# Kernel tuning notes

Hardware: AMD Instinct MI355X
Metric: run time of the kernel (lower is better)

The kernel has to match this reference:

```python
import jax, jax.numpy as jnp
import numpy as np

B, T, D, H, K = 2, 1024, 1024, 4096, 8


def setup_inputs() -> dict:
    key = jax.random.key(0)
    ks = jax.random.split(key, 5)
    x = jax.random.normal(ks[0], (B, T, D), dtype=jnp.float32)
    # hard one-hot routing weights per token (no learned router)
    expert_ids = jax.random.randint(ks[1], (B, T), 0, K)
    combine_weights = jax.nn.one_hot(expert_ids, K, dtype=jnp.float32)
    scale_in = 1.0 / np.sqrt(D)
    scale_h = 1.0 / np.sqrt(H)
    wg = jax.random.normal(ks[2], (K, D, H), dtype=jnp.float32) * scale_in
    wu = jax.random.normal(ks[3], (K, D, H), dtype=jnp.float32) * scale_in
    wd = jax.random.normal(ks[4], (K, H, D), dtype=jnp.float32) * scale_h
    return {"x": x, "combine_weights": combine_weights, "wg": wg, "wu": wu, "wd": wd}


def reference(x, combine_weights, wg, wu, wd):
    # Each expert is a SwiGLU FFN: down( silu(gate(x)) * up(x) ).
    # Dense baseline: every token runs through all K experts (as in source).
    g = jnp.einsum('btd,kdh->btkh', x, wg)          # [B,T,K,H]
    u = jnp.einsum('btd,kdh->btkh', x, wu)          # [B,T,K,H]
    h = jax.nn.silu(g) * u                          # [B,T,K,H]
    expert_outs = jnp.einsum('btkh,khd->btkd', h, wd)  # [B,T,K,D]
    y = jnp.einsum('btk,btkd->btd', combine_weights, expert_outs)
    return y.astype(x.dtype)
```

## Files before the change

kernel.cpp:

```cpp
#include <hip/hip_runtime.h>
#include <hip/hip_bf16.h>

typedef __attribute__((ext_vector_type(8))) short bf16x8;
typedef __attribute__((ext_vector_type(4))) float f32x4;
typedef unsigned short u16;

#define NTOK 2048
#define DDIM 1024
#define HDIM 4096
#define KEXP 8

#define BM 320
#define BK 64
#define NDESC 16

__device__ __forceinline__ u16 f2bf(float f) {
  __hip_bfloat16 b = __float2bfloat16(f);
  union { __hip_bfloat16 b; u16 u; } c; c.b = b; return c.u;
}
__device__ __forceinline__ unsigned pk2(float a, float b) {
  return (unsigned)f2bf(a) | ((unsigned)f2bf(b) << 16);
}

#define BAR() do { \
  asm volatile("s_waitcnt lgkmcnt(0)" ::: "memory"); \
  __builtin_amdgcn_sched_barrier(0); \
  __builtin_amdgcn_s_barrier(); \
  __builtin_amdgcn_sched_barrier(0); \
} while (0)

__global__ void route_kernel(const float* __restrict__ cw, int* __restrict__ offs,
                             int* __restrict__ perm, float* __restrict__ wsel,
                             int* __restrict__ desc) {
  __shared__ int cnt[KEXP];
  __shared__ int base[KEXP];
  const int t = threadIdx.x;
  if (t < KEXP) cnt[t] = 0;
  __syncthreads();
  int eid[8]; float wv[8];
  #pragma unroll
  for (int i = 0; i < 8; i++) {
    const int tok = t * 8 + i;
    const float* p = cw + tok * KEXP;
    int best = 0; float bw = p[0];
    #pragma unroll
    for (int k = 1; k < KEXP; k++) { float v = p[k]; if (v > bw) { bw = v; best = k; } }
    eid[i] = best; wv[i] = bw;
    atomicAdd(&cnt[best], 1);
  }
  __syncthreads();
  if (t == 0) {
    int s = 0, nd = 0;
    for (int k = 0; k < KEXP; k++) {
      const int ck = cnt[k];
      base[k] = s; offs[k] = s;
      for (int m0 = 0; m0 < ck && nd < NDESC; m0 += BM)
        desc[nd++] = (k << 12) | (s + m0);
      s += ck;
    }
    offs[KEXP] = s;
    for (; nd < NDESC; nd++) desc[nd] = -1;
  }
  __syncthreads();
  #pragma unroll
  for (int i = 0; i < 8; i++) {
    const int tok = t * 8 + i;
    const int pos = atomicAdd(&base[eid[i]], 1);
    perm[pos] = tok;
    wsel[pos] = wv[i];
  }
}

__global__ void gather_x(const float* __restrict__ x, const int* __restrict__ perm,
                         u16* __restrict__ Xb) {
  const int slot = blockIdx.x;
  const int tok = perm[slot];
  const int t = threadIdx.x;
  float4 v = ((const float4*)(x + (size_t)tok * DDIM))[t];
  ushort4 o; o.x = f2bf(v.x); o.y = f2bf(v.y); o.z = f2bf(v.z); o.w = f2bf(v.w);
  ((ushort4*)(Xb + (size_t)slot * DDIM))[t] = o;
}

__global__ __launch_bounds__(1024, 4) void gemm_swiglu(
    const u16* __restrict__ Xb,
    const float* __restrict__ wg, const float* __restrict__ wu,
    const int* __restrict__ offs, const int* __restrict__ desc,
    u16* __restrict__ Hb) {
  __shared__ u16 As[2][BM * 64];
  __shared__ u16 Bs[2][2][64 * 64];

  const int d = desc[blockIdx.y];
  if (d < 0) return;
  const int e = d >> 12;
  const int slot0 = d & 0xFFF;
  const int Msub = offs[e + 1] - slot0;
  const int mceil = min(BM, (Msub + 15) & ~15);
  const int n0 = blockIdx.x * 64;

  const int t = threadIdx.x;
  const int lane = t & 63;
  const int W = t >> 6;
  const int wm = W >> 2;
  const int wn = W & 3;
  const int l15 = lane & 15;
  const int lhi = lane >> 4;
  const int fm_lim = min(5, max(0, (Msub - wm * 80 + 15) >> 4));

  const int a_row = t >> 1;
  const bool do_a = (t < 640) && (a_row < mceil);
  const int a_c0 = (t & 1) * 4;
  const u16* a_src = Xb + (size_t)min(slot0 + a_row, NTOK - 1) * DDIM + a_c0 * 8;
  const int a_swz = a_row & 7;

  const int tb = t & 511;
  const int matsel = t >> 9;
  const float* b_base = (matsel ? wu : wg) + (size_t)e * DDIM * HDIM;
  const int b_n = tb & 63;
  const int b_c = tb >> 6;
  const float* b_src = b_base + (size_t)(b_c * 8) * HDIM + n0 + b_n;
  const int b_off = b_n * 64 + ((b_c ^ (b_n & 7)) << 3);

  float bR[8];
  uint4 aT0, aT1, aT2, aT3;
  f32x4 accg[5] = {};
  f32x4 accu[5] = {};

  #define AISSUE(tile) if (do_a) { const uint4* p_ = (const uint4*)(a_src + (tile) * BK); \
    aT0 = p_[0]; aT1 = p_[1]; aT2 = p_[2]; aT3 = p_[3]; }
  #define AWRITE(buf) if (do_a) { u16* base_ = &As[buf][a_row * 64]; \
    *(uint4*)(base_ + (((a_c0 + 0) ^ a_swz) << 3)) = aT0; \
    *(uint4*)(base_ + (((a_c0 + 1) ^ a_swz) << 3)) = aT1; \
    *(uint4*)(base_ + (((a_c0 + 2) ^ a_swz) << 3)) = aT2; \
    *(uint4*)(base_ + (((a_c0 + 3) ^ a_swz) << 3)) = aT3; }
  #define LOADB(tile) { const float* p_ = b_src + (size_t)(tile) * BK * HDIM; \
    _Pragma("unroll") for (int j = 0; j < 8; j++) bR[j] = p_[(size_t)j * HDIM]; }
  #define WRITEB(buf) { uint4 w_; \
    w_.x = pk2(bR[0], bR[1]); w_.y = pk2(bR[2], bR[3]); \
    w_.z = pk2(bR[4], bR[5]); w_.w = pk2(bR[6], bR[7]); \
    *(uint4*)(&Bs[buf][matsel][b_off]) = w_; }
  #define COMPUTE(buf) { _Pragma("unroll") for (int ks = 0; ks < 2; ks++) { \
      const int cx_ = (((ks << 2) + lhi) ^ (l15 & 7)) << 3; \
      bf16x8 bg_ = *(const bf16x8*)(&Bs[buf][0][(wn * 16 + l15) * 64] + cx_); \
      bf16x8 bu_ = *(const bf16x8*)(&Bs[buf][1][(wn * 16 + l15) * 64] + cx_); \
      _Pragma("unroll") for (int fm = 0; fm < 5; fm++) { \
        if (fm < fm_lim) { \
          bf16x8 af_ = *(const bf16x8*)(&As[buf][(wm * 80 + fm * 16 + l15) * 64] + cx_); \
          accg[fm] = __builtin_amdgcn_mfma_f32_16x16x32_bf16(af_, bg_, accg[fm], 0, 0, 0); \
          accu[fm] = __builtin_amdgcn_mfma_f32_16x16x32_bf16(af_, bu_, accu[fm], 0, 0, 0); } } } }

  LOADB(0);
  AISSUE(0);
  WRITEB(0);
  LOADB(1);
  AWRITE(0);
  BAR();

  #pragma unroll 1
  for (int it = 0; it < 16; it += 2) {
    if (it + 1 < 16) AISSUE(it + 1);
    __builtin_amdgcn_sched_barrier(0);
    COMPUTE(0);
    if (it + 1 < 16) {
      WRITEB(1);
      if (it + 2 < 16) LOADB(it + 2);
      AWRITE(1);
    }
    BAR();
    if (it + 2 < 16) AISSUE(it + 2);
    __builtin_amdgcn_sched_barrier(0);
    COMPUTE(1);
    if (it + 2 < 16) {
      WRITEB(0);
      if (it + 3 < 16) LOADB(it + 3);
      AWRITE(0);
    }
    BAR();
  }
  #undef AISSUE
  #undef AWRITE
  #undef LOADB
  #undef WRITEB
  #undef COMPUTE

  #pragma unroll
  for (int fm = 0; fm < 5; fm++) {
    #pragma unroll
    for (int i = 0; i < 4; i++) {
      const int row = wm * 80 + fm * 16 + lhi * 4 + i;
      if (row < Msub) {
        const float g = accg[fm][i];
        const float u = accu[fm][i];
        const float h = (g / (1.0f + __expf(-g))) * u;
        Hb[(size_t)(slot0 + row) * HDIM + n0 + wn * 16 + l15] = f2bf(h);
      }
    }
  }
}

__global__ __launch_bounds__(1024, 4) void gemm_down(
    const u16* __restrict__ Hb, const float* __restrict__ wd,
    const int* __restrict__ offs, const int* __restrict__ desc,
    const int* __restrict__ perm, const float* __restrict__ wsel,
    float* __restrict__ y) {
  __shared__ u16 As[2][BM * 64];
  __shared__ u16 Bs[2][128 * 64];

  const int d = desc[blockIdx.y];
  if (d < 0) return;
  const int e = d >> 12;
  const int slot0 = d & 0xFFF;
  const int Msub = offs[e + 1] - slot0;
  const int mceil = min(BM, (Msub + 15) & ~15);
  const int n0 = blockIdx.x * 128;
  const int kbase = blockIdx.z * (HDIM / 4);

  const float* Wd = wd + (size_t)e * HDIM * DDIM;

  const int t = threadIdx.x;
  const int lane = t & 63;
  const int W = t >> 6;
  const int wm = W >> 2;
  const int wn = W & 3;
  const int l15 = lane & 15;
  const int lhi = lane >> 4;
  const int fm_lim = min(5, max(0, (Msub - wm * 80 + 15) >> 4));

  const int a_row = t >> 1;
  const bool do_a = (t < 640) && (a_row < mceil);
  const int a_c0 = (t & 1) * 4;
  const u16* a_src = Hb + (size_t)min(slot0 + a_row, NTOK - 1) * HDIM + kbase + a_c0 * 8;
  const int a_swz = a_row & 7;

  const int b_n = t & 127;
  const int b_c = t >> 7;
  const float* b_src = Wd + (size_t)(kbase + b_c * 8) * DDIM + n0 + b_n;
  const int b_off = b_n * 64 + ((b_c ^ (b_n & 7)) << 3);

  float bR[8];
  uint4 aT0, aT1, aT2, aT3;
  f32x4 acc[5][2] = {};

  #define AISSUE(tile) if (do_a) { const uint4* p_ = (const uint4*)(a_src + (tile) * BK); \
    aT0 = p_[0]; aT1 = p_[1]; aT2 = p_[2]; aT3 = p_[3]; }
  #define AWRITE(buf) if (do_a) { u16* base_ = &As[buf][a_row * 64]; \
    *(uint4*)(base_ + (((a_c0 + 0) ^ a_swz) << 3)) = aT0; \
    *(uint4*)(base_ + (((a_c0 + 1) ^ a_swz) << 3)) = aT1; \
    *(uint4*)(base_ + (((a_c0 + 2) ^ a_swz) << 3)) = aT2; \
    *(uint4*)(base_ + (((a_c0 + 3) ^ a_swz) << 3)) = aT3; }
  #define LOADB(tile) { const float* p_ = b_src + (size_t)(tile) * BK * DDIM; \
    _Pragma("unroll") for (int j = 0; j < 8; j++) bR[j] = p_[(size_t)j * DDIM]; }
  #define WRITEB(buf) { uint4 w_; \
    w_.x = pk2(bR[0], bR[1]); w_.y = pk2(bR[2], bR[3]); \
    w_.z = pk2(bR[4], bR[5]); w_.w = pk2(bR[6], bR[7]); \
    *(uint4*)(&Bs[buf][b_off]) = w_; }
  #define COMPUTE(buf) { _Pragma("unroll") for (int ks = 0; ks < 2; ks++) { \
      const int cx_ = (((ks << 2) + lhi) ^ (l15 & 7)) << 3; \
      bf16x8 bf0_ = *(const bf16x8*)(&Bs[buf][(wn * 32 + l15) * 64] + cx_); \
      bf16x8 bf1_ = *(const bf16x8*)(&Bs[buf][(wn * 32 + 16 + l15) * 64] + cx_); \
      _Pragma("unroll") for (int fm = 0; fm < 5; fm++) { \
        if (fm < fm_lim) { \
          bf16x8 af_ = *(const bf16x8*)(&As[buf][(wm * 80 + fm * 16 + l15) * 64] + cx_); \
          acc[fm][0] = __builtin_amdgcn_mfma_f32_16x16x32_bf16(af_, bf0_, acc[fm][0], 0, 0, 0); \
          acc[fm][1] = __builtin_amdgcn_mfma_f32_16x16x32_bf16(af_, bf1_, acc[fm][1], 0, 0, 0); } } } }

  LOADB(0);
  AISSUE(0);
  WRITEB(0);
  LOADB(1);
  AWRITE(0);
  BAR();

  #pragma unroll 1
  for (int it = 0; it < 16; it += 2) {
    if (it + 1 < 16) AISSUE(it + 1);
    __builtin_amdgcn_sched_barrier(0);
    COMPUTE(0);
    if (it + 1 < 16) {
      WRITEB(1);
      if (it + 2 < 16) LOADB(it + 2);
      AWRITE(1);
    }
    BAR();
    if (it + 2 < 16) AISSUE(it + 2);
    __builtin_amdgcn_sched_barrier(0);
    COMPUTE(1);
    if (it + 2 < 16) {
      WRITEB(0);
      if (it + 3 < 16) LOADB(it + 3);
      AWRITE(0);
    }
    BAR();
  }
  #undef AISSUE
  #undef AWRITE
  #undef LOADB
  #undef WRITEB
  #undef COMPUTE

  #pragma unroll
  for (int fm = 0; fm < 5; fm++) {
    #pragma unroll
    for (int i = 0; i < 4; i++) {
      const int row = wm * 80 + fm * 16 + lhi * 4 + i;
      if (row < Msub) {
        const int slot = slot0 + row;
        const int tok = perm[slot];
        const float w = wsel[slot];
        const size_t base = (size_t)tok * DDIM + n0 + wn * 32;
        atomicAdd(y + base + l15, acc[fm][0][i] * w);
        atomicAdd(y + base + 16 + l15, acc[fm][1][i] * w);
      }
    }
  }
}

extern "C" void kernel_launch(void* const* d_in, const int* in_sizes, int n_in,
                              void* d_out, int out_size, void* d_ws, size_t ws_size,
                              hipStream_t stream) {
  const float* x  = (const float*)d_in[0];
  const float* cw = (const float*)d_in[1];
  const float* wg = (const float*)d_in[2];
  const float* wu = (const float*)d_in[3];
  const float* wd = (const float*)d_in[4];
  float* y = (float*)d_out;

  char* ws = (char*)d_ws;
  int* offs   = (int*)ws;
  int* desc   = (int*)(ws + 64);
  int* perm   = (int*)(ws + 128);
  float* wsel = (float*)(ws + 128 + NTOK * 4);
  u16* Xb = (u16*)(ws + 32768);
  u16* Hb = (u16*)(ws + 32768 + (size_t)NTOK * DDIM * 2);

  hipMemsetAsync(d_out, 0, (size_t)NTOK * DDIM * sizeof(float), stream);
  route_kernel<<<1, 256, 0, stream>>>(cw, offs, perm, wsel, desc);
  gather_x<<<NTOK, 256, 0, stream>>>(x, perm, Xb);
  gemm_swiglu<<<dim3(HDIM / 64, NDESC), 1024, 0, stream>>>(Xb, wg, wu, offs, desc, Hb);
  gemm_down<<<dim3(DDIM / 128, NDESC, 4), 1024, 0, stream>>>(Hb, wd, offs, desc, perm, wsel, y);
}
```

Measured before the change: 151.6 us.

## Load A tiles directly global-to-LDS with pre-swizzled activation layouts

Replaces the register-staged A-tile loads (global to VGPR, then ds_write) in both GEMM kernels with global_load_lds direct copies into shared memory. Since direct LDS loads cannot apply a per-row swizzle on write, the producers (gather_x and the SwiGLU epilogue) now store activations with the XOR swizzle already applied in global memory, and the compute reads use a slot-based swizzle. Barriers now wait on vmcnt so the async copies are complete before use. This is meant to cut VGPR pressure and LDS write instructions, in exchange for coupling the global layout to the kernel's tile shape and relying on precise vmcnt counts for correctness.

```diff
diff --git a/kernel.cpp b/kernel.cpp
--- a/kernel.cpp
+++ b/kernel.cpp
@@ -22,8 +22,8 @@
   return (unsigned)f2bf(a) | ((unsigned)f2bf(b) << 16);
 }
 
-#define BAR() do { \
-  asm volatile("s_waitcnt lgkmcnt(0)" ::: "memory"); \
+#define BARV(N) do { \
+  asm volatile("s_waitcnt lgkmcnt(0) vmcnt(" #N ")" ::: "memory"); \
   __builtin_amdgcn_sched_barrier(0); \
   __builtin_amdgcn_s_barrier(); \
   __builtin_amdgcn_sched_barrier(0); \
@@ -76,9 +76,12 @@
   const int slot = blockIdx.x;
   const int tok = perm[slot];
   const int t = threadIdx.x;
+  const int s7 = slot & 7;
   float4 v = ((const float4*)(x + (size_t)tok * DDIM))[t];
   ushort4 o; o.x = f2bf(v.x); o.y = f2bf(v.y); o.z = f2bf(v.z); o.w = f2bf(v.w);
-  ((ushort4*)(Xb + (size_t)slot * DDIM))[t] = o;
+  const int c = t >> 1;
+  const int cp = (c & ~7) | ((c & 7) ^ s7);
+  *(ushort4*)(Xb + (size_t)slot * DDIM + cp * 8 + (t & 1) * 4) = o;
 }
 
 __global__ __launch_bounds__(1024, 4) void gemm_swiglu(
@@ -94,7 +97,6 @@
   const int e = d >> 12;
   const int slot0 = d & 0xFFF;
   const int Msub = offs[e + 1] - slot0;
-  const int mceil = min(BM, (Msub + 15) & ~15);
   const int n0 = blockIdx.x * 64;
 
   const int t = threadIdx.x;
@@ -105,12 +107,7 @@
   const int l15 = lane & 15;
   const int lhi = lane >> 4;
   const int fm_lim = min(5, max(0, (Msub - wm * 80 + 15) >> 4));
-
-  const int a_row = t >> 1;
-  const bool do_a = (t < 640) && (a_row < mceil);
-  const int a_c0 = (t & 1) * 4;
-  const u16* a_src = Xb + (size_t)min(slot0 + a_row, NTOK - 1) * DDIM + a_c0 * 8;
-  const int a_swz = a_row & 7;
+  const int asw = (slot0 + l15) & 7;
 
   const int tb = t & 511;
   const int matsel = t >> 9;
@@ -121,17 +118,20 @@
   const int b_off = b_n * 64 + ((b_c ^ (b_n & 7)) << 3);
 
   float bR[8];
-  uint4 aT0, aT1, aT2, aT3;
   f32x4 accg[5] = {};
   f32x4 accu[5] = {};
 
-  #define AISSUE(tile) if (do_a) { const uint4* p_ = (const uint4*)(a_src + (tile) * BK); \
-    aT0 = p_[0]; aT1 = p_[1]; aT2 = p_[2]; aT3 = p_[3]; }
-  #define AWRITE(buf) if (do_a) { u16* base_ = &As[buf][a_row * 64]; \
-    *(uint4*)(base_ + (((a_c0 + 0) ^ a_swz) << 3)) = aT0; \
-    *(uint4*)(base_ + (((a_c0 + 1) ^ a_swz) << 3)) = aT1; \
-    *(uint4*)(base_ + (((a_c0 + 2) ^ a_swz) << 3)) = aT2; \
-    *(uint4*)(base_ + (((a_c0 + 3) ^ a_swz) << 3)) = aT3; }
+  #define AGLOAD(tile, buf) if (t < 640) { \
+    _Pragma("unroll") for (int j = 0; j < 4; j++) { \
+      const int q_ = j * 640 + t; \
+      const int row_ = q_ >> 3; \
+      const u16* src_ = Xb + (size_t)min(slot0 + row_, NTOK - 1) * DDIM \
+                        + (tile) * BK + (q_ & 7) * 8; \
+      __builtin_amdgcn_global_load_lds( \
+        (const __attribute__((address_space(1))) unsigned int*)src_, \
+        (__attribute__((address_space(3))) unsigned int*)(&As[buf][0] + q_ * 8), \
+        16, 0, 0); \
+    } }
   #define LOADB(tile) { const float* p_ = b_src + (size_t)(tile) * BK * HDIM; \
     _Pragma("unroll") for (int j = 0; j < 8; j++) bR[j] = p_[(size_t)j * HDIM]; }
   #define WRITEB(buf) { uint4 w_; \
@@ -139,45 +139,42 @@
     w_.z = pk2(bR[4], bR[5]); w_.w = pk2(bR[6], bR[7]); \
     *(uint4*)(&Bs[buf][matsel][b_off]) = w_; }
   #define COMPUTE(buf) { _Pragma("unroll") for (int ks = 0; ks < 2; ks++) { \
-      const int cx_ = (((ks << 2) + lhi) ^ (l15 & 7)) << 3; \
-      bf16x8 bg_ = *(const bf16x8*)(&Bs[buf][0][(wn * 16 + l15) * 64] + cx_); \
-      bf16x8 bu_ = *(const bf16x8*)(&Bs[buf][1][(wn * 16 + l15) * 64] + cx_); \
+      const int cb_ = (((ks << 2) + lhi) ^ (l15 & 7)) << 3; \
+      const int ca_ = (((ks << 2) + lhi) ^ asw) << 3; \
+      bf16x8 bg_ = *(const bf16x8*)(&Bs[buf][0][(wn * 16 + l15) * 64] + cb_); \
+      bf16x8 bu_ = *(const bf16x8*)(&Bs[buf][1][(wn * 16 + l15) * 64] + cb_); \
       _Pragma("unroll") for (int fm = 0; fm < 5; fm++) { \
         if (fm < fm_lim) { \
-          bf16x8 af_ = *(const bf16x8*)(&As[buf][(wm * 80 + fm * 16 + l15) * 64] + cx_); \
+          bf16x8 af_ = *(const bf16x8*)(&As[buf][(wm * 80 + fm * 16 + l15) * 64] + ca_); \
           accg[fm] = __builtin_amdgcn_mfma_f32_16x16x32_bf16(af_, bg_, accg[fm], 0, 0, 0); \
           accu[fm] = __builtin_amdgcn_mfma_f32_16x16x32_bf16(af_, bu_, accu[fm], 0, 0, 0); } } } }
 
   LOADB(0);
-  AISSUE(0);
+  AGLOAD(0, 0);
   WRITEB(0);
   LOADB(1);
-  AWRITE(0);
-  BAR();
+  BARV(8);
 
   #pragma unroll 1
   for (int it = 0; it < 16; it += 2) {
-    if (it + 1 < 16) AISSUE(it + 1);
+    if (it + 1 < 16) AGLOAD(it + 1, 1);
     __builtin_amdgcn_sched_barrier(0);
     COMPUTE(0);
     if (it + 1 < 16) {
       WRITEB(1);
       if (it + 2 < 16) LOADB(it + 2);
-      AWRITE(1);
-    }
-    BAR();
-    if (it + 2 < 16) AISSUE(it + 2);
+    }
+    if (it + 2 < 16) BARV(8); else BARV(0);
+    if (it + 2 < 16) AGLOAD(it + 2, 0);
     __builtin_amdgcn_sched_barrier(0);
     COMPUTE(1);
     if (it + 2 < 16) {
       WRITEB(0);
       if (it + 3 < 16) LOADB(it + 3);
-      AWRITE(0);
-    }
-    BAR();
-  }
-  #undef AISSUE
-  #undef AWRITE
+    }
+    if (it + 3 < 16) BARV(8); else BARV(0);
+  }
+  #undef AGLOAD
   #undef LOADB
   #undef WRITEB
   #undef COMPUTE
@@ -191,7 +188,8 @@
         const float g = accg[fm][i];
         const float u = accu[fm][i];
         const float h = (g / (1.0f + __expf(-g))) * u;
-        Hb[(size_t)(slot0 + row) * HDIM + n0 + wn * 16 + l15] = f2bf(h);
+        const int s7 = (slot0 + row) & 7;
+        Hb[(size_t)(slot0 + row) * HDIM + ((n0 + wn * 16 + l15) ^ (s7 << 3))] = f2bf(h);
       }
     }
   }
@@ -210,7 +208,6 @@
   const int e = d >> 12;
   const int slot0 = d & 0xFFF;
   const int Msub = offs[e + 1] - slot0;
-  const int mceil = min(BM, (Msub + 15) & ~15);
   const int n0 = blockIdx.x * 128;
   const int kbase = blockIdx.z * (HDIM / 4);
 
@@ -224,12 +221,7 @@
   const int l15 = lane & 15;
   const int lhi = lane >> 4;
   const int fm_lim = min(5, max(0, (Msub - wm * 80 + 15) >> 4));
-
-  const int a_row = t >> 1;
-  const bool do_a = (t < 640) && (a_row < mceil);
-  const int a_c0 = (t & 1) * 4;
-  const u16* a_src = Hb + (size_t)min(slot0 + a_row, NTOK - 1) * HDIM + kbase + a_c0 * 8;
-  const int a_swz = a_row & 7;
+  const int asw = (slot0 + l15) & 7;
 
   const int b_n = t & 127;
   const int b_c = t >> 7;
@@ -237,16 +229,19 @@
   const int b_off = b_n * 64 + ((b_c ^ (b_n & 7)) << 3);
 
   float bR[8];
-  uint4 aT0, aT1, aT2, aT3;
   f32x4 acc[5][2] = {};
 
-  #define AISSUE(tile) if (do_a) { const uint4* p_ = (const uint4*)(a_src + (tile) * BK); \
-    aT0 = p_[0]; aT1 = p_[1]; aT2 = p_[2]; aT3 = p_[3]; }
-  #define AWRITE(buf) if (do_a) { u16* base_ = &As[buf][a_row * 64]; \
-    *(uint4*)(base_ + (((a_c0 + 0) ^ a_swz) << 3)) = aT0; \
-    *(uint4*)(base_ + (((a_c0 + 1) ^ a_swz) << 3)) = aT1; \
-    *(uint4*)(base_ + (((a_c0 + 2) ^ a_swz) << 3)) = aT2; \
-    *(uint4*)(base_ + (((a_c0 + 3) ^ a_swz) << 3)) = aT3; }
+  #define AGLOAD(tile, buf) if (t < 640) { \
+    _Pragma("unroll") for (int j = 0; j < 4; j++) { \
+      const int q_ = j * 640 + t; \
+      const int row_ = q_ >> 3; \
+      const u16* src_ = Hb + (size_t)min(slot0 + row_, NTOK - 1) * HDIM \
+                        + kbase + (tile) * BK + (q_ & 7) * 8; \
+      __builtin_amdgcn_global_load_lds( \
+        (const __attribute__((address_space(1))) unsigned int*)src_, \
+        (__attribute__((address_space(3))) unsigned int*)(&As[buf][0] + q_ * 8), \
+        16, 0, 0); \
+    } }
   #define LOADB(tile) { const float* p_ = b_src + (size_t)(tile) * BK * DDIM; \
     _Pragma("unroll") for (int j = 0; j < 8; j++) bR[j] = p_[(size_t)j * DDIM]; }
   #define WRITEB(buf) { uint4 w_; \
@@ -254,45 +249,42 @@
     w_.z = pk2(bR[4], bR[5]); w_.w = pk2(bR[6], bR[7]); \
     *(uint4*)(&Bs[buf][b_off]) = w_; }
   #define COMPUTE(buf) { _Pragma("unroll") for (int ks = 0; ks < 2; ks++) { \
-      const int cx_ = (((ks << 2) + lhi) ^ (l15 & 7)) << 3; \
-      bf16x8 bf0_ = *(const bf16x8*)(&Bs[buf][(wn * 32 + l15) * 64] + cx_); \
-      bf16x8 bf1_ = *(const bf16x8*)(&Bs[buf][(wn * 32 + 16 + l15) * 64] + cx_); \
+      const int cb_ = (((ks << 2) + lhi) ^ (l15 & 7)) << 3; \
+      const int ca_ = (((ks << 2) + lhi) ^ asw) << 3; \
+      bf16x8 bf0_ = *(const bf16x8*)(&Bs[buf][(wn * 32 + l15) * 64] + cb_); \
+      bf16x8 bf1_ = *(const bf16x8*)(&Bs[buf][(wn * 32 + 16 + l15) * 64] + cb_); \
       _Pragma("unroll") for (int fm = 0; fm < 5; fm++) { \
         if (fm < fm_lim) { \
-          bf16x8 af_ = *(const bf16x8*)(&As[buf][(wm * 80 + fm * 16 + l15) * 64] + cx_); \
+          bf16x8 af_ = *(const bf16x8*)(&As[buf][(wm * 80 + fm * 16 + l15) * 64] + ca_); \
           acc[fm][0] = __builtin_amdgcn_mfma_f32_16x16x32_bf16(af_, bf0_, acc[fm][0], 0, 0, 0); \
           acc[fm][1] = __builtin_amdgcn_mfma_f32_16x16x32_bf16(af_, bf1_, acc[fm][1], 0, 0, 0); } } } }
 
   LOADB(0);
-  AISSUE(0);
+  AGLOAD(0, 0);
   WRITEB(0);
   LOADB(1);
-  AWRITE(0);
-  BAR();
+  BARV(8);
 
   #pragma unroll 1
   for (int it = 0; it < 16; it += 2) {
-    if (it + 1 < 16) AISSUE(it + 1);
+    if (it + 1 < 16) AGLOAD(it + 1, 1);
     __builtin_amdgcn_sched_barrier(0);
     COMPUTE(0);
     if (it + 1 < 16) {
       WRITEB(1);
       if (it + 2 < 16) LOADB(it + 2);
-      AWRITE(1);
-    }
-    BAR();
-    if (it + 2 < 16) AISSUE(it + 2);
+    }
+    if (it + 2 < 16) BARV(8); else BARV(0);
+    if (it + 2 < 16) AGLOAD(it + 2, 0);
     __builtin_amdgcn_sched_barrier(0);
     COMPUTE(1);
     if (it + 2 < 16) {
       WRITEB(0);
       if (it + 3 < 16) LOADB(it + 3);
-      AWRITE(0);
-    }
-    BAR();
-  }
-  #undef AISSUE
-  #undef AWRITE
+    }
+    if (it + 3 < 16) BARV(8); else BARV(0);
+  }
+  #undef AGLOAD
   #undef LOADB
   #undef WRITEB
   #undef COMPUTE
```

Result: no change. 151.6 us (+0.0%).
